# Kernel tuning notes

Hardware: AMD Instinct MI355X
Metric: run time of the kernel (lower is better)

Reference implementation:

```python
import jax, jax.numpy as jnp
import numpy as np
from jax import lax

# Static model/config sizes
B, ANG, C, H, NF, NB = 1, 9, 3, 128, 16, 2


def get_freq_position(n):
    """Anti-diagonal frequency bands of an n x n angular-DCT grid (python/static)."""
    bands = []
    for i in range(n):
        bands.append(([i], [0]))
    for j in range(1, n):
        bands.append(([n - 1], [j]))
    for item in bands:
        while item[0][0] > 0 and item[1][0] < n - 1:
            item[0].insert(0, item[0][0] - 1)
            item[1].insert(0, item[1][0] + 1)
    return bands


def dct_mat(n):
    """Orthonormal DCT-II matrix (row k = k-th basis)."""
    k = jnp.arange(n, dtype=jnp.float32)[:, None]
    i = jnp.arange(n, dtype=jnp.float32)[None, :]
    m = jnp.cos(jnp.pi * (i + 0.5) * k / n) * jnp.sqrt(2.0 / n)
    return m.at[0].multiply(1.0 / np.sqrt(2.0))


def conv3d(x, w, b):
    # x: (N, Cin, D, H, W), w: (Cout, Cin, 3, 3, 3)
    y = lax.conv_general_dilated(x, w, (1, 1, 1), 'SAME',
                                 dimension_numbers=('NCDHW', 'OIDHW', 'NCDHW'))
    return y + b[None, :, None, None, None]


def branch(cut, wi, bi, a, wb, bb):
    """init conv + NB ResBlock3D (PReLU -> Conv3d, residual), plus outer skip."""
    y0 = conv3d(cut, wi, bi)
    y = y0
    for k in range(NB):
        r = jnp.where(y >= 0, y, a[k] * y)  # PReLU (single-parameter)
        y = y + conv3d(r, wb[k], bb[k])
    return y0 + y


def setup_inputs() -> dict:
    key = jax.random.key(0)
    ks = jax.random.split(key, 32)

    def nrm(k, shape, s=0.05):
        return jax.random.normal(k, shape, dtype=jnp.float32) * s

    inp = {"x": jax.random.normal(ks[0], (B, ANG, ANG, C, H, H), dtype=jnp.float32)}
    i = 1
    for n in ("dc", "lo", "mi", "hi"):
        inp[f"w_{n}_i"] = nrm(ks[i], (NF, C, 3, 3, 3)); i += 1
        inp[f"b_{n}_i"] = nrm(ks[i], (NF,)); i += 1
        inp[f"a_{n}"] = jnp.full((NB,), 0.25, dtype=jnp.float32)
        inp[f"w_{n}"] = nrm(ks[i], (NB, NF, NF, 3, 3, 3)); i += 1
        inp[f"b_{n}"] = nrm(ks[i], (NB, NF)); i += 1
    inp["w_last"] = nrm(ks[i], (C, NF))  # 1x1 Conv2d, no bias
    return inp


def reference(x, w_dc_i, b_dc_i, a_dc, w_dc, b_dc,
              w_lo_i, b_lo_i, a_lo, w_lo, b_lo,
              w_mi_i, b_mi_i, a_mi, w_mi, b_mi,
              w_hi_i, b_hi_i, a_hi, w_hi, b_hi, w_last):
    b, u, v, c, h, w = x.shape
    Da = dct_mat(u)  # angular DCT (u == v)
    Ds = dct_mat(h)  # spatial DCT (h == w)

    # SpaAngDCT: spatial 2D DCT then angular 2D DCT
    xf = jnp.einsum('buvchw,Hh,Ww->buvcHW', x, Ds, Ds)
    xf = jnp.einsum('buvchw,Uu,Vv->bUVchw', xf, Da, Da)

    x_rec = jnp.zeros((b, NF, u, v, h, w), dtype=x.dtype)
    for idx, (ui, vi) in enumerate(get_freq_position(u)):
        if idx == 0:
            p = (w_dc_i, b_dc_i, a_dc, w_dc, b_dc)
        elif idx <= 2:
            p = (w_lo_i, b_lo_i, a_lo, w_lo, b_lo)
        elif idx <= u - 1:
            p = (w_mi_i, b_mi_i, a_mi, w_mi, b_mi)
        else:
            p = (w_hi_i, b_hi_i, a_hi, w_hi, b_hi)
        ua, va = jnp.array(ui), jnp.array(vi)
        cut = xf[:, ua, va].transpose(0, 2, 1, 3, 4)  # (b, c, L, h, w)
        out = branch(cut, *p)                          # (b, NF, L, h, w)
        x_rec = x_rec.at[:, :, ua, va].set(out)        # scatter band back

    # 'b c u v h w -> b c (u h) (v w)' then 1x1 conv (NF -> 3)
    xr = x_rec.transpose(0, 1, 2, 4, 3, 5).reshape(b, NF, u * h, v * w)
    xr = jnp.einsum('bnHW,on->boHW', xr, w_last)
    xr = xr.reshape(b, c, u, h, v, w).transpose(0, 2, 4, 1, 3, 5)  # (b,u,v,c,h,w)

    # InverseSpaAngDCT: angular IDCT then spatial IDCT
    xr = jnp.einsum('bUVchw,Uu,Vv->buvchw', xr, Da, Da)
    xr = jnp.einsum('buvcHW,Hh,Ww->buvchw', xr, Ds, Ds)
    return xr + x
```

## Files before the change

### kernel.cpp

```cpp
#include <hip/hip_runtime.h>
#include <hip/hip_bf16.h>
#include <math.h>

typedef __hip_bfloat16 bf16;
typedef __attribute__((ext_vector_type(8))) short short8;
typedef __attribute__((ext_vector_type(4))) float floatx4;
typedef __attribute__((ext_vector_type(4))) unsigned int uint4v;
typedef __attribute__((ext_vector_type(2))) unsigned int uint2v;

#define HW 16384
#define NSLICE 243

__constant__ int c_s_of_p[81] = {
  0, 1,1, 2,2,2, 3,3,3,3, 4,4,4,4,4, 5,5,5,5,5,5, 6,6,6,6,6,6,6,
  7,7,7,7,7,7,7,7, 8,8,8,8,8,8,8,8,8, 9,9,9,9,9,9,9,9,
  10,10,10,10,10,10,10, 11,11,11,11,11,11, 12,12,12,12,12,
  13,13,13,13, 14,14,14, 15,15, 16};
__constant__ int c_l_of_p[81] = {
  0, 0,1, 0,1,2, 0,1,2,3, 0,1,2,3,4, 0,1,2,3,4,5, 0,1,2,3,4,5,6,
  0,1,2,3,4,5,6,7, 0,1,2,3,4,5,6,7,8, 0,1,2,3,4,5,6,7,
  0,1,2,3,4,5,6, 0,1,2,3,4,5, 0,1,2,3,4, 0,1,2,3, 0,1,2, 0,1, 0};
__constant__ int c_L_of_s[17] = {1,2,3,4,5,6,7,8,9,8,7,6,5,4,3,2,1};
__constant__ int c_g_of_s[17] = {0,1,1,2,2,2,2,2,2,3,3,3,3,3,3,3,3};
__constant__ int c_pos_uv[81] = {
  0,1,3,6,10,15,21,28,36,
  2,4,7,11,16,22,29,37,45,
  5,8,12,17,23,30,38,46,53,
  9,13,18,24,31,39,47,54,60,
  14,19,25,32,40,48,55,61,66,
  20,26,33,41,49,56,62,67,71,
  27,34,42,50,57,63,68,72,75,
  35,43,51,58,64,69,73,76,78,
  44,52,59,65,70,74,77,79,80};

struct WPtrs {
  const float* wi[4]; const float* bi[4]; const float* a[4];
  const float* wb[4]; const float* bb[4]; const float* wl;
};

__device__ __forceinline__ unsigned short f2bf(float f) {
  return __bfloat16_as_ushort(__float2bfloat16(f));
}
__device__ __forceinline__ float bf2f(unsigned short u) {
  return __uint_as_float(((unsigned int)u) << 16);
}
__device__ __forceinline__ float bflo(unsigned int w) {
  return __uint_as_float(w << 16);
}
__device__ __forceinline__ float bfhi(unsigned int w) {
  return __uint_as_float(w & 0xffff0000u);
}
__device__ __forceinline__ unsigned int pack2(float a, float b) {
  return (unsigned int)f2bf(a) | ((unsigned int)f2bf(b) << 16);
}
__device__ __forceinline__ float invprelu(float v, float invA) {
  return (v >= 0.f) ? v : v * invA;
}
__device__ __forceinline__ void bfsplit(float v, unsigned short& hi, unsigned short& lo) {
  unsigned int bits = __float_as_uint(v);
  hi = (unsigned short)(bits >> 16);
  lo = f2bf(v - __uint_as_float(bits & 0xffff0000u));
}
__device__ __forceinline__ void gl_lds16(const void* g, void* l) {
  __builtin_amdgcn_global_load_lds(
      (const __attribute__((address_space(1))) unsigned int*)g,
      (__attribute__((address_space(3))) unsigned int*)l, 16, 0, 0);
}
__device__ __forceinline__ int ldsoff(int plane, int col) {
  return plane * 2112 + ((plane & 3) << 5) + (col << 4);
}
__device__ __forceinline__ void wmf_repack(const WPtrs& P, unsigned short* Wmf, int t) {
  if (t >= 92160) return;
  int s = t / 7680, r = t % 7680;
  int step = r / 512, r2 = r % 512;
  int lane = r2 >> 3, j = r2 & 7;
  int d = step / 5, i = step % 5;
  int q = lane >> 4, m = lane & 15;
  int tl = 2 * i + (q >> 1);
  int cin = (q & 1) * 8 + j;
  float val = 0.f;
  if (tl <= 8) {
    int ky = tl / 3, kx = tl % 3;
    int tap = d * 9 + ky * 3 + kx;
    if (s < 4) {
      if (cin < 3) val = P.wi[s][(m * 3 + cin) * 27 + tap];
    } else {
      int g = (s - 4) >> 1, k = (s - 4) & 1;
      val = P.wb[g][((k * 16 + m) * 16 + cin) * 27 + tap];
    }
  }
  Wmf[t] = f2bf(val);
}

__global__ __launch_bounds__(256) void k_init(WPtrs P, float* DaF,
                                              unsigned short* TFhi, unsigned short* TFlo,
                                              unsigned short* TIhi, unsigned short* TIlo,
                                              float* BiF, float* BbF,
                                              float* AF, float* WlF) {
  const double PI = 3.14159265358979323846;
  int t = blockIdx.x * 256 + threadIdx.x;
  if (t < 81) {
    int U = t / 9, u = t % 9;
    double d = cos(PI * (u + 0.5) * U / 9.0) * sqrt(2.0 / 9.0);
    if (U == 0) d *= (1.0 / sqrt(2.0));
    DaF[t] = (float)d;
  }
  if (t < 16384) {
    int jj = t & 7, lane = (t >> 3) & 63, ks = (t >> 9) & 3, tile = t >> 11;
    int row = tile * 16 + (lane & 15);
    int colk = ks * 32 + (lane >> 4) * 8 + jj;
    double vF = cos(PI * (colk + 0.5) * row / 128.0) * sqrt(2.0 / 128.0);
    if (row == 0) vF *= (1.0 / sqrt(2.0));
    double vI = cos(PI * (row + 0.5) * colk / 128.0) * sqrt(2.0 / 128.0);
    if (colk == 0) vI *= (1.0 / sqrt(2.0));
    unsigned short h, l;
    bfsplit((float)vF, h, l); TFhi[t] = h; TFlo[t] = l;
    bfsplit((float)vI, h, l); TIhi[t] = h; TIlo[t] = l;
  }
  if (t < 64)  BiF[t] = P.bi[t / 16][t % 16];
  if (t < 128) BbF[t] = P.bb[t / 32][t % 32];
  if (t < 8)   AF[t]  = P.a[t / 2][t % 2];
  if (t < 48)  WlF[t] = P.wl[t];
}

__global__ __launch_bounds__(1024) void k_dct2(const float* __restrict__ X,
                                               const unsigned short* __restrict__ tabhi,
                                               const unsigned short* __restrict__ tablo,
                                               const float* __restrict__ xres,
                                               float* __restrict__ Yf,
                                               unsigned short* __restrict__ Ybf,
                                               WPtrs P,
                                               unsigned short* __restrict__ Wmf) {
  if (blockIdx.x >= 243) {
    int t2 = (blockIdx.x - 243) * 1024 + threadIdx.x;
    wmf_repack(P, Wmf, t2);
    return;
  }
  __shared__ unsigned short sThi[128 * 136];
  __shared__ unsigned short sTlo[128 * 136];
  int s = blockIdx.x;
  int t = threadIdx.x;
  int lane = t & 63, wv16 = t >> 6;
  int mt8 = wv16 & 7, nh = wv16 >> 3;
  int q = lane >> 4, n16 = lane & 15;
  const float* Xs = X + (size_t)s * HW;

  floatx4 acc[4];
#pragma unroll
  for (int ntl = 0; ntl < 4; ntl++) acc[ntl] = (floatx4){0.f, 0.f, 0.f, 0.f};

#pragma unroll
  for (int ks = 0; ks < 4; ks++) {
    short8 ahi, alo;
    {
      const float* xp = Xs + (mt8 * 16 + n16) * 128 + ks * 32 + q * 8;
      float4 a = *(const float4*)xp;
      float4 b = *(const float4*)(xp + 4);
      union { short8 v; unsigned short u[8]; } H, L;
      float xv[8] = {a.x, a.y, a.z, a.w, b.x, b.y, b.z, b.w};
#pragma unroll
      for (int j = 0; j < 8; j++) bfsplit(xv[j], H.u[j], L.u[j]);
      ahi = H.v; alo = L.v;
    }
#pragma unroll
    for (int ntl = 0; ntl < 4; ntl++) {
      int e = (nh * 4 + ntl) * 2048 + ks * 512 + lane * 8;
      short8 bh = *(const short8*)(tabhi + e);
      short8 bl = *(const short8*)(tablo + e);
      acc[ntl] = __builtin_amdgcn_mfma_f32_16x16x32_bf16(ahi, bl, acc[ntl], 0, 0, 0);
      acc[ntl] = __builtin_amdgcn_mfma_f32_16x16x32_bf16(alo, bh, acc[ntl], 0, 0, 0);
      acc[ntl] = __builtin_amdgcn_mfma_f32_16x16x32_bf16(ahi, bh, acc[ntl], 0, 0, 0);
    }
  }

#pragma unroll
  for (int ntl = 0; ntl < 4; ntl++) {
    int col = (nh * 4 + ntl) * 16 + n16;
    int rowb = mt8 * 16 + q * 4;
#pragma unroll
    for (int rp = 0; rp < 4; rp += 2) {
      unsigned short h0, l0, h1, l1;
      bfsplit(acc[ntl][rp], h0, l0);
      bfsplit(acc[ntl][rp + 1], h1, l1);
      int widx = (col * 136 + rowb + rp) >> 1;
      ((unsigned int*)sThi)[widx] = (unsigned int)h0 | ((unsigned int)h1 << 16);
      ((unsigned int*)sTlo)[widx] = (unsigned int)l0 | ((unsigned int)l1 << 16);
    }
  }
  __syncthreads();

#pragma unroll
  for (int ntl = 0; ntl < 4; ntl++) acc[ntl] = (floatx4){0.f, 0.f, 0.f, 0.f};

#pragma unroll
  for (int ks = 0; ks < 4; ks++) {
    int e0 = mt8 * 2048 + ks * 512 + lane * 8;
    short8 ahi = *(const short8*)(tabhi + e0);
    short8 alo = *(const short8*)(tablo + e0);
#pragma unroll
    for (int ntl = 0; ntl < 4; ntl++) {
      int off = ((nh * 4 + ntl) * 16 + n16) * 136 + ks * 32 + q * 8;
      short8 bh = *(const short8*)(sThi + off);
      short8 bl = *(const short8*)(sTlo + off);
      acc[ntl] = __builtin_amdgcn_mfma_f32_16x16x32_bf16(ahi, bl, acc[ntl], 0, 0, 0);
      acc[ntl] = __builtin_amdgcn_mfma_f32_16x16x32_bf16(alo, bh, acc[ntl], 0, 0, 0);
      acc[ntl] = __builtin_amdgcn_mfma_f32_16x16x32_bf16(ahi, bh, acc[ntl], 0, 0, 0);
    }
  }

#pragma unroll
  for (int ntl = 0; ntl < 4; ntl++) {
    int row0 = mt8 * 16 + q * 4;
    int col = (nh * 4 + ntl) * 16 + n16;
#pragma unroll
    for (int r = 0; r < 4; r++) {
      size_t oi = (size_t)s * HW + (size_t)(row0 + r) * 128 + col;
      float v = acc[ntl][r];
      if (Ybf) {
        Ybf[oi] = f2bf(v);
      } else {
        if (xres) v += xres[oi];
        Yf[oi] = v;
      }
    }
  }
}

__global__ __launch_bounds__(256) void k_angfwd(const unsigned short* __restrict__ in,
                                                const float* __restrict__ DaF,
                                                unsigned short* __restrict__ out) {
  __shared__ float sDa[81];
  int t = threadIdx.x;
  if (t < 81) sDa[t] = DaF[t];
  __syncthreads();
  int idx = blockIdx.x * 256 + t;
  int hw = idx & (HW - 1);
  int r = idx >> 14;
  int c = r % 3, ub = r / 3;
  unsigned short raw[81];
#pragma unroll
  for (int u = 0; u < 9; u++)
#pragma unroll
    for (int v = 0; v < 9; v++)
      raw[u * 9 + v] = in[(size_t)((u * 9 + v) * 3 + c) * HW + hw];
  float tmp[3][9];
#pragma unroll
  for (int i = 0; i < 3; i++)
#pragma unroll
    for (int v = 0; v < 9; v++) tmp[i][v] = 0.f;
#pragma unroll
  for (int u = 0; u < 9; u++) {
    float fv[9];
#pragma unroll
    for (int v = 0; v < 9; v++) fv[v] = bf2f(raw[u * 9 + v]);
#pragma unroll
    for (int i = 0; i < 3; i++) {
      float dc = sDa[(ub * 3 + i) * 9 + u];
#pragma unroll
      for (int v = 0; v < 9; v++) tmp[i][v] += dc * fv[v];
    }
  }
#pragma unroll
  for (int i = 0; i < 3; i++) {
    int U = ub * 3 + i;
#pragma unroll
    for (int V = 0; V < 9; V++) {
      float acc = 0.f;
#pragma unroll
      for (int v = 0; v < 9; v++) acc += sDa[V * 9 + v] * tmp[i][v];
      out[(size_t)(c_pos_uv[U * 9 + V] * 3 + c) * HW + hw] = f2bf(acc);
    }
  }
}

__global__ __launch_bounds__(256) void k_anginv(const float* __restrict__ xrb,
                                                const float* __restrict__ DaF,
                                                float* __restrict__ out) {
  __shared__ float sDa[81];
  int t = threadIdx.x;
  if (t < 81) sDa[t] = DaF[t];
  __syncthreads();
  int idx = blockIdx.x * 256 + t;
  int hw = idx & (HW - 1);
  int r = idx >> 14;
  int c = r % 3, ub = r / 3;
  float raw[81];
#pragma unroll
  for (int U = 0; U < 9; U++)
#pragma unroll
    for (int V = 0; V < 9; V++)
      raw[U * 9 + V] = xrb[((size_t)c_pos_uv[U * 9 + V] * 3 + c) * HW + hw];
  float tmp[3][9];
#pragma unroll
  for (int i = 0; i < 3; i++)
#pragma unroll
    for (int V = 0; V < 9; V++) tmp[i][V] = 0.f;
#pragma unroll
  for (int U = 0; U < 9; U++) {
#pragma unroll
    for (int i = 0; i < 3; i++) {
      float dc = sDa[U * 9 + (ub * 3 + i)];
#pragma unroll
      for (int V = 0; V < 9; V++) tmp[i][V] += dc * raw[U * 9 + V];
    }
  }
#pragma unroll
  for (int i = 0; i < 3; i++) {
    int u = ub * 3 + i;
#pragma unroll
    for (int v = 0; v < 9; v++) {
      float acc = 0.f;
#pragma unroll
      for (int V = 0; V < 9; V++) acc += sDa[V * 9 + v] * tmp[i][V];
      out[(size_t)((u * 9 + v) * 3 + c) * HW + hw] = acc;
    }
  }
}

__global__ __launch_bounds__(1024, 8) void k_conv(const unsigned short* __restrict__ src,
                                              const unsigned short* __restrict__ prevAct,
                                              const unsigned short* __restrict__ act0,
                                              const unsigned short* __restrict__ Wmf,
                                              const float* __restrict__ BiF,
                                              const float* __restrict__ BbF,
                                              const float* __restrict__ AF,
                                              const float* __restrict__ WlF,
                                              int sel,
                                              unsigned short* __restrict__ boutAct,
                                              float* __restrict__ xrbOut) {
  __shared__ unsigned short s_lds[21184];
  int p = blockIdx.y;
  int s = c_s_of_p[p], l = c_l_of_p[p];
  int g = c_g_of_s[s], Ls = c_L_of_s[s];
  int row0 = blockIdx.x * 8;
  int t = threadIdx.x;
  int lane = t & 63, wv16 = t >> 6;
  int row8 = wv16 & 7, ch = wv16 >> 3;
  int q = lane >> 4, n = lane & 15;

  float aNext = (sel < 2) ? AF[g * 2 + sel] : 0.f;
  float invA  = (sel > 0) ? 1.0f / AF[g * 2 + sel - 1] : 0.f;

  {
    uint4v z = (uint4v){0u, 0u, 0u, 0u};
    int zmax = (sel == 0) ? 1320 : 40;
    for (int i = t; i < zmax; i += 1024) {
      int row, half, col;
      if (i < 40) { row = i >> 2; half = (i >> 1) & 1; col = (i & 1) ? 129 : 0; }
      else { int j = i - 40; row = j >> 7; col = (j & 127) + 1; half = 1; }
      *(uint4v*)((char*)s_lds + ldsoff(row * 2 + half, col)) = z;
    }
    for (int row = 0; row < 10; row++) {
      int grow = row0 - 1 + row;
      if ((unsigned)grow >= 128u) {
        for (int i = t; i < 264; i += 1024) {
          int half = i / 132, col = i % 132;
          *(uint4v*)((char*)s_lds + ldsoff(row * 2 + half, col)) = z;
        }
      }
    }
  }

  int off2[5];
#pragma unroll
  for (int i = 0; i < 5; i++) {
    int tl = 2 * i + (q >> 1);
    if (tl > 8) tl = 8;
    int ky = tl / 3, kx = tl % 3;
    off2[i] = ldsoff(2 * (row8 + ky) + (q & 1), n + kx) + ch * 1024;
  }

  int setIdx = (sel == 0) ? g : (4 + g * 2 + (sel - 1));
  const char* WsetBase = (const char*)Wmf + (size_t)setIdx * 15 * 1024;

  floatx4 acc[4];
#pragma unroll
  for (int cg = 0; cg < 4; cg++) acc[cg] = (floatx4){0.f, 0.f, 0.f, 0.f};

  const int dord[3] = {0, 2, 1};
  for (int k = 0; k < 3; k++) {
    int d = dord[k];
    int l2 = l + d - 1;
    if (l2 < 0 || l2 >= Ls) continue;
    int p2 = p + d - 1;
    __syncthreads();
    if (sel == 0) {
#pragma unroll
      for (int it = 0; it < 2; it++) {
        int id = t + it * 1024;
        if (id < 1280) {
          int row = id >> 7, col = id & 127;
          int grow = row0 - 1 + row;
          if ((unsigned)grow < 128u) {
            const unsigned short* s0 = src + (size_t)p2 * 3 * HW +
                                       (size_t)grow * 128 + col;
            unsigned int c0 = s0[0];
            unsigned int c1 = s0[HW];
            unsigned int c2 = s0[2 * HW];
            uint4v val;
            val.x = c0 | (c1 << 16);
            val.y = c2;
            val.z = 0u; val.w = 0u;
            *(uint4v*)((char*)s_lds + ldsoff(row * 2, col + 1)) = val;
          }
        }
      }
    } else {
#pragma unroll
      for (int it = 0; it < 3; it++) {
        int id = t + it * 1024;
        if (id < 2560) {
          int row = id >> 8, half = (id >> 7) & 1, col = id & 127;
          int grow = row0 - 1 + row;
          if ((unsigned)grow < 128u) {
            const void* gp = (const void*)(src +
                (((size_t)p2 * HW + (size_t)grow * 128 + col) * 16 + half * 8));
            void* lp = (void*)((char*)s_lds + ldsoff(row * 2 + half, col + 1));
            gl_lds16(gp, lp);
          }
        }
      }
    }
    __syncthreads();
    short8 af[5];
#pragma unroll
    for (int i = 0; i < 5; i++)
      af[i] = *(const short8*)(WsetBase + ((d * 5 + i) * 64 + lane) * 16);
#pragma unroll
    for (int cg = 0; cg < 4; cg++) {
#pragma unroll
      for (int i = 0; i < 5; i++) {
        short8 b = *(const short8*)((const char*)s_lds + off2[i] + cg * 256);
        acc[cg] = __builtin_amdgcn_mfma_f32_16x16x32_bf16(af[i], b, acc[cg], 0, 0, 0);
      }
    }
  }

  const float* bp = (sel == 0) ? (BiF + g * 16) : (BbF + g * 32 + (sel - 1) * 16);
  float bz[4];
#pragma unroll
  for (int r = 0; r < 4; r++) bz[r] = bp[q * 4 + r];
  int h = row0 + row8;

  if (sel < 2) {
#pragma unroll
    for (int cg = 0; cg < 4; cg++) {
      size_t pix = (size_t)p * HW + h * 128 + ch * 64 + cg * 16 + n;
      float r0 = acc[cg][0] + bz[0], r1 = acc[cg][1] + bz[1];
      float r2 = acc[cg][2] + bz[2], r3 = acc[cg][3] + bz[3];
      if (sel != 0) {
        uint2v pv = *(const uint2v*)((const char*)s_lds +
            ldsoff(2 * (row8 + 1) + (q >> 1), ch * 64 + cg * 16 + n + 1) + (q & 1) * 8);
        r0 += invprelu(bflo(pv.x), invA); r1 += invprelu(bfhi(pv.x), invA);
        r2 += invprelu(bflo(pv.y), invA); r3 += invprelu(bfhi(pv.y), invA);
      }
      r0 = fmaxf(r0, 0.f) + aNext * fminf(r0, 0.f);
      r1 = fmaxf(r1, 0.f) + aNext * fminf(r1, 0.f);
      r2 = fmaxf(r2, 0.f) + aNext * fminf(r2, 0.f);
      r3 = fmaxf(r3, 0.f) + aNext * fminf(r3, 0.f);
      uint2v ov; ov.x = pack2(r0, r1); ov.y = pack2(r2, r3);
      *(uint2v*)(boutAct + pix * 16 + q * 4) = ov;
    }
  } else {
    float invA0 = 1.0f / AF[g * 2];
    float wl0[4], wl1[4], wl2[4];
#pragma unroll
    for (int r = 0; r < 4; r++) {
      wl0[r] = WlF[q * 4 + r];
      wl1[r] = WlF[16 + q * 4 + r];
      wl2[r] = WlF[32 + q * 4 + r];
    }
#pragma unroll
    for (int cg = 0; cg < 4; cg++) {
      size_t pix = (size_t)p * HW + h * 128 + ch * 64 + cg * 16 + n;
      float r0 = acc[cg][0] + bz[0], r1 = acc[cg][1] + bz[1];
      float r2 = acc[cg][2] + bz[2], r3 = acc[cg][3] + bz[3];
      uint2v pv = *(const uint2v*)((const char*)s_lds +
          ldsoff(2 * (row8 + 1) + (q >> 1), ch * 64 + cg * 16 + n + 1) + (q & 1) * 8);
      r0 += invprelu(bflo(pv.x), invA); r1 += invprelu(bfhi(pv.x), invA);
      r2 += invprelu(bflo(pv.y), invA); r3 += invprelu(bfhi(pv.y), invA);
      uint2v p0 = *(const uint2v*)(act0 + pix * 16 + q * 4);
      r0 += invprelu(bflo(p0.x), invA0); r1 += invprelu(bfhi(p0.x), invA0);
      r2 += invprelu(bflo(p0.y), invA0); r3 += invprelu(bfhi(p0.y), invA0);
      float o0 = wl0[0] * r0 + wl0[1] * r1 + wl0[2] * r2 + wl0[3] * r3;
      float o1 = wl1[0] * r0 + wl1[1] * r1 + wl1[2] * r2 + wl1[3] * r3;
      float o2 = wl2[0] * r0 + wl2[1] * r1 + wl2[2] * r2 + wl2[3] * r3;
      o0 += __shfl_xor(o0, 16); o0 += __shfl_xor(o0, 32);
      o1 += __shfl_xor(o1, 16); o1 += __shfl_xor(o1, 32);
      o2 += __shfl_xor(o2, 16); o2 += __shfl_xor(o2, 32);
      if (q == 0) {
        size_t hw = (size_t)h * 128 + ch * 64 + cg * 16 + n;
        xrbOut[((size_t)p * 3 + 0) * HW + hw] = o0;
        xrbOut[((size_t)p * 3 + 1) * HW + hw] = o1;
        xrbOut[((size_t)p * 3 + 2) * HW + hw] = o2;
      }
    }
  }
}

extern "C" void kernel_launch(void* const* d_in, const int* in_sizes, int n_in,
                              void* d_out, int out_size, void* d_ws, size_t ws_size,
                              hipStream_t stream) {
  (void)in_sizes; (void)n_in; (void)out_size; (void)ws_size;
  const float* x = (const float*)d_in[0];
  WPtrs P;
  for (int g = 0; g < 4; g++) {
    int b = 1 + g * 5;
    P.wi[g] = (const float*)d_in[b + 0];
    P.bi[g] = (const float*)d_in[b + 1];
    P.a[g]  = (const float*)d_in[b + 2];
    P.wb[g] = (const float*)d_in[b + 3];
    P.bb[g] = (const float*)d_in[b + 4];
  }
  P.wl = (const float*)d_in[21];

  char* base = (char*)d_ws;
  size_t off = 0;
  auto take = [&](size_t bytes) -> char* {
    char* r = base + off;
    off += (bytes + 255) & ~(size_t)255;
    return r;
  };
  float* DaF = (float*)take(81 * 4);
  unsigned short* TFhi = (unsigned short*)take(16384 * 2);
  unsigned short* TFlo = (unsigned short*)take(16384 * 2);
  unsigned short* TIhi = (unsigned short*)take(16384 * 2);
  unsigned short* TIlo = (unsigned short*)take(16384 * 2);
  unsigned short* Wmf = (unsigned short*)take(92160 * 2);
  float* BiF   = (float*)take(256);
  float* BbF   = (float*)take(512);
  float* AF    = (float*)take(32);
  float* WlF   = (float*)take(192);
  float* R1 = (float*)take((size_t)NSLICE * HW * 4);
  unsigned short* B1 = (unsigned short*)take((size_t)NSLICE * HW * 2);
  float* R3 = (float*)take((size_t)NSLICE * HW * 4);
  unsigned short* braw0 = (unsigned short*)take((size_t)81 * 16 * HW * 2);
  unsigned short* braw1 = (unsigned short*)take((size_t)81 * 16 * HW * 2);
  unsigned short* xf2b = (unsigned short*)R3;
  float* xrb = R3;

  k_init<<<64, 256, 0, stream>>>(P, DaF, TFhi, TFlo, TIhi, TIlo,
                                 BiF, BbF, AF, WlF);
  k_dct2<<<333, 1024, 0, stream>>>(x, TFhi, TFlo, nullptr, nullptr, B1, P, Wmf);
  k_angfwd<<<576, 256, 0, stream>>>(B1, DaF, xf2b);
  k_conv<<<dim3(16, 81), 1024, 0, stream>>>(xf2b, nullptr, nullptr, Wmf,
                                            BiF, BbF, AF, WlF, 0, braw0, nullptr);
  k_conv<<<dim3(16, 81), 1024, 0, stream>>>(braw0, braw0, nullptr, Wmf,
                                            BiF, BbF, AF, WlF, 1, braw1, nullptr);
  k_conv<<<dim3(16, 81), 1024, 0, stream>>>(braw1, braw1, braw0, Wmf,
                                            BiF, BbF, AF, WlF, 2, nullptr, xrb);
  k_anginv<<<576, 256, 0, stream>>>(xrb, DaF, R1);
  k_dct2<<<243, 1024, 0, stream>>>(R1, TIhi, TIlo, x, (float*)d_out, nullptr, P, Wmf);
}
```

Before: 264.8 us.

## Drop init kernel; compute DCT tables in-kernel into LDS, read params directly

Removes the separate k_init launch. Each k_dct2 block now builds its 128x128 DCT basis (split into hi/lo bf16) in LDS with float cosf on an integer-reduced angle. The angular DCT coefficients are built on the fly in k_angfwd and k_anginv, and k_conv reads biases, PReLU slopes and last-layer weights straight from the input pointers. This saves one kernel launch and the table traffic through global memory, but adds per-block transcendental work and a 132KB dynamic LDS allocation, which limits k_dct2 to one block per CU and may lose some table precision versus the double-precision build.

```diff
diff --git a/kernel.cpp b/kernel.cpp
--- a/kernel.cpp
+++ b/kernel.cpp
@@ -69,6 +69,12 @@
 __device__ __forceinline__ int ldsoff(int plane, int col) {
   return plane * 2112 + ((plane & 3) << 5) + (col << 4);
 }
+__device__ __forceinline__ float da_entry(int t) {
+  int U = t / 9, u = t % 9;
+  if (U == 0) return 0.33333334f;
+  int m9 = (U * (2 * u + 1)) % 36;
+  return cosf((float)m9 * 0.17453293f) * 0.47140452f;
+}
 __device__ __forceinline__ void wmf_repack(const WPtrs& P, unsigned short* Wmf, int t) {
   if (t >= 92160) return;
   int s = t / 7680, r = t % 7680;
@@ -92,40 +98,7 @@
   Wmf[t] = f2bf(val);
 }
 
-__global__ __launch_bounds__(256) void k_init(WPtrs P, float* DaF,
-                                              unsigned short* TFhi, unsigned short* TFlo,
-                                              unsigned short* TIhi, unsigned short* TIlo,
-                                              float* BiF, float* BbF,
-                                              float* AF, float* WlF) {
-  const double PI = 3.14159265358979323846;
-  int t = blockIdx.x * 256 + threadIdx.x;
-  if (t < 81) {
-    int U = t / 9, u = t % 9;
-    double d = cos(PI * (u + 0.5) * U / 9.0) * sqrt(2.0 / 9.0);
-    if (U == 0) d *= (1.0 / sqrt(2.0));
-    DaF[t] = (float)d;
-  }
-  if (t < 16384) {
-    int jj = t & 7, lane = (t >> 3) & 63, ks = (t >> 9) & 3, tile = t >> 11;
-    int row = tile * 16 + (lane & 15);
-    int colk = ks * 32 + (lane >> 4) * 8 + jj;
-    double vF = cos(PI * (colk + 0.5) * row / 128.0) * sqrt(2.0 / 128.0);
-    if (row == 0) vF *= (1.0 / sqrt(2.0));
-    double vI = cos(PI * (row + 0.5) * colk / 128.0) * sqrt(2.0 / 128.0);
-    if (colk == 0) vI *= (1.0 / sqrt(2.0));
-    unsigned short h, l;
-    bfsplit((float)vF, h, l); TFhi[t] = h; TFlo[t] = l;
-    bfsplit((float)vI, h, l); TIhi[t] = h; TIlo[t] = l;
-  }
-  if (t < 64)  BiF[t] = P.bi[t / 16][t % 16];
-  if (t < 128) BbF[t] = P.bb[t / 32][t % 32];
-  if (t < 8)   AF[t]  = P.a[t / 2][t % 2];
-  if (t < 48)  WlF[t] = P.wl[t];
-}
-
 __global__ __launch_bounds__(1024) void k_dct2(const float* __restrict__ X,
-                                               const unsigned short* __restrict__ tabhi,
-                                               const unsigned short* __restrict__ tablo,
                                                const float* __restrict__ xres,
                                                float* __restrict__ Yf,
                                                unsigned short* __restrict__ Ybf,
@@ -136,14 +109,32 @@
     wmf_repack(P, Wmf, t2);
     return;
   }
-  __shared__ unsigned short sThi[128 * 136];
-  __shared__ unsigned short sTlo[128 * 136];
+  extern __shared__ char dynlds[];
+  unsigned short* sThi = (unsigned short*)dynlds;
+  unsigned short* sTlo = (unsigned short*)(dynlds + 34816);
+  unsigned short* sBhi = (unsigned short*)(dynlds + 69632);
+  unsigned short* sBlo = (unsigned short*)(dynlds + 102400);
   int s = blockIdx.x;
   int t = threadIdx.x;
   int lane = t & 63, wv16 = t >> 6;
   int mt8 = wv16 & 7, nh = wv16 >> 3;
   int q = lane >> 4, n16 = lane & 15;
   const float* Xs = X + (size_t)s * HW;
+  int isFwd = (Ybf != nullptr);
+
+  for (int i = t; i < 16384; i += 1024) {
+    int jj = i & 7, ln = (i >> 3) & 63, ks = (i >> 9) & 3, tile = i >> 11;
+    int row = tile * 16 + (ln & 15);
+    int colk = ks * 32 + (ln >> 4) * 8 + jj;
+    int mm = isFwd ? (row * (2 * colk + 1)) & 511
+                   : (colk * (2 * row + 1)) & 511;
+    float vv = cosf((float)mm * 0.012271846f) * 0.125f;
+    if (isFwd ? (row == 0) : (colk == 0)) vv *= 0.70710678f;
+    unsigned short hh, ll;
+    bfsplit(vv, hh, ll);
+    sBhi[i] = hh; sBlo[i] = ll;
+  }
+  __syncthreads();
 
   floatx4 acc[4];
 #pragma unroll
@@ -165,8 +156,8 @@
 #pragma unroll
     for (int ntl = 0; ntl < 4; ntl++) {
       int e = (nh * 4 + ntl) * 2048 + ks * 512 + lane * 8;
-      short8 bh = *(const short8*)(tabhi + e);
-      short8 bl = *(const short8*)(tablo + e);
+      short8 bh = *(const short8*)(sBhi + e);
+      short8 bl = *(const short8*)(sBlo + e);
       acc[ntl] = __builtin_amdgcn_mfma_f32_16x16x32_bf16(ahi, bl, acc[ntl], 0, 0, 0);
       acc[ntl] = __builtin_amdgcn_mfma_f32_16x16x32_bf16(alo, bh, acc[ntl], 0, 0, 0);
       acc[ntl] = __builtin_amdgcn_mfma_f32_16x16x32_bf16(ahi, bh, acc[ntl], 0, 0, 0);
@@ -195,8 +186,8 @@
 #pragma unroll
   for (int ks = 0; ks < 4; ks++) {
     int e0 = mt8 * 2048 + ks * 512 + lane * 8;
-    short8 ahi = *(const short8*)(tabhi + e0);
-    short8 alo = *(const short8*)(tablo + e0);
+    short8 ahi = *(const short8*)(sBhi + e0);
+    short8 alo = *(const short8*)(sBlo + e0);
 #pragma unroll
     for (int ntl = 0; ntl < 4; ntl++) {
       int off = ((nh * 4 + ntl) * 16 + n16) * 136 + ks * 32 + q * 8;
@@ -227,11 +218,10 @@
 }
 
 __global__ __launch_bounds__(256) void k_angfwd(const unsigned short* __restrict__ in,
-                                                const float* __restrict__ DaF,
                                                 unsigned short* __restrict__ out) {
   __shared__ float sDa[81];
   int t = threadIdx.x;
-  if (t < 81) sDa[t] = DaF[t];
+  if (t < 81) sDa[t] = da_entry(t);
   __syncthreads();
   int idx = blockIdx.x * 256 + t;
   int hw = idx & (HW - 1);
@@ -274,11 +264,10 @@
 }
 
 __global__ __launch_bounds__(256) void k_anginv(const float* __restrict__ xrb,
-                                                const float* __restrict__ DaF,
                                                 float* __restrict__ out) {
   __shared__ float sDa[81];
   int t = threadIdx.x;
-  if (t < 81) sDa[t] = DaF[t];
+  if (t < 81) sDa[t] = da_entry(t);
   __syncthreads();
   int idx = blockIdx.x * 256 + t;
   int hw = idx & (HW - 1);
@@ -318,13 +307,9 @@
 }
 
 __global__ __launch_bounds__(1024, 8) void k_conv(const unsigned short* __restrict__ src,
-                                              const unsigned short* __restrict__ prevAct,
                                               const unsigned short* __restrict__ act0,
                                               const unsigned short* __restrict__ Wmf,
-                                              const float* __restrict__ BiF,
-                                              const float* __restrict__ BbF,
-                                              const float* __restrict__ AF,
-                                              const float* __restrict__ WlF,
+                                              WPtrs P,
                                               int sel,
                                               unsigned short* __restrict__ boutAct,
                                               float* __restrict__ xrbOut) {
@@ -338,8 +323,8 @@
   int row8 = wv16 & 7, ch = wv16 >> 3;
   int q = lane >> 4, n = lane & 15;
 
-  float aNext = (sel < 2) ? AF[g * 2 + sel] : 0.f;
-  float invA  = (sel > 0) ? 1.0f / AF[g * 2 + sel - 1] : 0.f;
+  float aNext = (sel < 2) ? P.a[g][sel] : 0.f;
+  float invA  = (sel > 0) ? 1.0f / P.a[g][sel - 1] : 0.f;
 
   {
     uint4v z = (uint4v){0u, 0u, 0u, 0u};
@@ -436,7 +421,7 @@
     }
   }
 
-  const float* bp = (sel == 0) ? (BiF + g * 16) : (BbF + g * 32 + (sel - 1) * 16);
+  const float* bp = (sel == 0) ? P.bi[g] : (P.bb[g] + (sel - 1) * 16);
   float bz[4];
 #pragma unroll
   for (int r = 0; r < 4; r++) bz[r] = bp[q * 4 + r];
@@ -462,13 +447,13 @@
       *(uint2v*)(boutAct + pix * 16 + q * 4) = ov;
     }
   } else {
-    float invA0 = 1.0f / AF[g * 2];
+    float invA0 = 1.0f / P.a[g][0];
     float wl0[4], wl1[4], wl2[4];
 #pragma unroll
     for (int r = 0; r < 4; r++) {
-      wl0[r] = WlF[q * 4 + r];
-      wl1[r] = WlF[16 + q * 4 + r];
-      wl2[r] = WlF[32 + q * 4 + r];
+      wl0[r] = P.wl[q * 4 + r];
+      wl1[r] = P.wl[16 + q * 4 + r];
+      wl2[r] = P.wl[32 + q * 4 + r];
     }
 #pragma unroll
     for (int cg = 0; cg < 4; cg++) {
@@ -521,16 +506,7 @@
     off += (bytes + 255) & ~(size_t)255;
     return r;
   };
-  float* DaF = (float*)take(81 * 4);
-  unsigned short* TFhi = (unsigned short*)take(16384 * 2);
-  unsigned short* TFlo = (unsigned short*)take(16384 * 2);
-  unsigned short* TIhi = (unsigned short*)take(16384 * 2);
-  unsigned short* TIlo = (unsigned short*)take(16384 * 2);
   unsigned short* Wmf = (unsigned short*)take(92160 * 2);
-  float* BiF   = (float*)take(256);
-  float* BbF   = (float*)take(512);
-  float* AF    = (float*)take(32);
-  float* WlF   = (float*)take(192);
   float* R1 = (float*)take((size_t)NSLICE * HW * 4);
   unsigned short* B1 = (unsigned short*)take((size_t)NSLICE * HW * 2);
   float* R3 = (float*)take((size_t)NSLICE * HW * 4);
@@ -539,16 +515,14 @@
   unsigned short* xf2b = (unsigned short*)R3;
   float* xrb = R3;
 
-  k_init<<<64, 256, 0, stream>>>(P, DaF, TFhi, TFlo, TIhi, TIlo,
-                                 BiF, BbF, AF, WlF);
-  k_dct2<<<333, 1024, 0, stream>>>(x, TFhi, TFlo, nullptr, nullptr, B1, P, Wmf);
-  k_angfwd<<<576, 256, 0, stream>>>(B1, DaF, xf2b);
-  k_conv<<<dim3(16, 81), 1024, 0, stream>>>(xf2b, nullptr, nullptr, Wmf,
-                                            BiF, BbF, AF, WlF, 0, braw0, nullptr);
-  k_conv<<<dim3(16, 81), 1024, 0, stream>>>(braw0, braw0, nullptr, Wmf,
-                                            BiF, BbF, AF, WlF, 1, braw1, nullptr);
-  k_conv<<<dim3(16, 81), 1024, 0, stream>>>(braw1, braw1, braw0, Wmf,
-                                            BiF, BbF, AF, WlF, 2, nullptr, xrb);
-  k_anginv<<<576, 256, 0, stream>>>(xrb, DaF, R1);
-  k_dct2<<<243, 1024, 0, stream>>>(R1, TIhi, TIlo, x, (float*)d_out, nullptr, P, Wmf);
-}
+  k_dct2<<<333, 1024, 135168, stream>>>(x, nullptr, nullptr, B1, P, Wmf);
+  k_angfwd<<<576, 256, 0, stream>>>(B1, xf2b);
+  k_conv<<<dim3(16, 81), 1024, 0, stream>>>(xf2b, nullptr, Wmf, P,
+                                            0, braw0, nullptr);
+  k_conv<<<dim3(16, 81), 1024, 0, stream>>>(braw0, nullptr, Wmf, P,
+                                            1, braw1, nullptr);
+  k_conv<<<dim3(16, 81), 1024, 0, stream>>>(braw1, braw0, Wmf, P,
+                                            2, nullptr, xrb);
+  k_anginv<<<576, 256, 0, stream>>>(xrb, R1);
+  k_dct2<<<243, 1024, 135168, stream>>>(R1, x, (float*)d_out, nullptr, P, Wmf);
+}
```

Result: no change. 264.6 us (median of 2 runs) (-0.1%).
